# Optimization experiments

Measured on AMD Instinct MI355X. Metric: run time of the kernel, lower is better.

## Reference

```python
import jax, jax.numpy as jnp
import numpy as np

B, C, N = 2, 128, 784  # batch, channels, spatial tokens (28x28)
TEMPERATURE = 11.313708498984761  # sqrt(C)


def setup_inputs() -> dict:
    key = jax.random.key(0)
    kq, kk, kv = jax.random.split(key, 3)
    q = jax.random.normal(kq, (B, C, N), dtype=jnp.float32)
    k = jax.random.normal(kk, (B, C, N), dtype=jnp.float32)
    v = jax.random.normal(kv, (B, C, N), dtype=jnp.float32)
    return {"q": q, "k": k, "v": v}


def reference(q, k, v):
    # dist_func == 'l1' branch of ScaledDotProductAttention (eval mode, dropout=0)
    qs = q / TEMPERATURE                                   # [B, C, Nq]
    # torch: q.unsqueeze(2).repeat -> [B,C,Nk,Nq]; k.unsqueeze(3).repeat -> [B,C,Nk,Nq]
    # broadcast instead of repeat; mean over channel dim 1
    diff = jnp.abs(qs[:, :, None, :] - k[:, :, :, None])   # [B, C, Nk, Nq]
    attn = jnp.mean(diff, axis=1)                          # [B, Nk, Nq]
    attn = jax.nn.softmax(attn, axis=-1)                   # softmax over Nq (last dim)
    # torch.bmm(v, attn.permute(0,2,1)): out[b,c,k] = sum_q v[b,c,q] * attn[b,k,q]
    out = jnp.einsum("bcq,bkq->bck", v, attn)              # [B, C, Nk]
    return (out, attn)
```

## Files before the change

kernel.cpp:

```cpp
#include <hip/hip_runtime.h>
#include <math.h>

constexpr int kB = 2;
constexpr int kC = 128;
constexpr int kN = 784;
constexpr float kInvT = 1.0f / 11.313708498984761f;
constexpr float kInvC = 1.0f / 128.0f;

constexpr size_t kOutElems  = (size_t)kB * kC * kN;
constexpr size_t kAttnElems = (size_t)kB * kN * kN;

__device__ inline float wave_max(float v) {
#pragma unroll
    for (int o = 32; o > 0; o >>= 1) v = fmaxf(v, __shfl_xor(v, o, 64));
    return v;
}
__device__ inline float wave_sum(float v) {
#pragma unroll
    for (int o = 32; o > 0; o >>= 1) v += __shfl_xor(v, o, 64);
    return v;
}

constexpr int TK = 64;
constexpr int TQ = 64;
constexpr int NKT = (kN + TK - 1) / TK;
constexpr int NQT = (kN + TQ - 1) / TQ;
constexpr int CSP = 2;
constexpr int CH = kC / CSP;
constexpr int DSTR = 68;

template <bool USE_WS>
__global__ __launch_bounds__(256) void dist_kernel(const float* __restrict__ qg,
                                                   const float* __restrict__ kg,
                                                   float* __restrict__ D0,
                                                   float* __restrict__ D1) {
    int bid = blockIdx.x;
    const int qt = bid % NQT; bid /= NQT;
    const int kt = bid % NKT; bid /= NKT;
    const int ch = bid & 1;   bid >>= 1;
    const int b  = bid;
    const int k0 = kt * TK;
    const int q0 = qt * TQ;
    const int t  = threadIdx.x;

    __shared__ float ks[CH][DSTR];
    __shared__ float qs[CH][DSTR];

    const float* kb = kg + ((size_t)b * kC + ch * CH) * kN;
    const float* qb = qg + ((size_t)b * kC + ch * CH) * kN;

#pragma unroll
    for (int i = t; i < CH * 16; i += 256) {
        const int c  = i >> 4;
        const int x4 = (i & 15) << 2;
        *reinterpret_cast<float4*>(&ks[c][x4]) =
            *reinterpret_cast<const float4*>(kb + (size_t)c * kN + min(k0 + x4, kN - 4));
        float4 qv = *reinterpret_cast<const float4*>(qb + (size_t)c * kN + min(q0 + x4, kN - 4));
        qv.x *= kInvT; qv.y *= kInvT; qv.z *= kInvT; qv.w *= kInvT;
        *reinterpret_cast<float4*>(&qs[c][x4]) = qv;
    }
    __syncthreads();

    const int qx = (t & 15) << 2;
    const int kx = (t >> 4) << 2;

    float acc[4][4];
#pragma unroll
    for (int i = 0; i < 4; ++i)
#pragma unroll
        for (int j = 0; j < 4; ++j) acc[i][j] = 0.0f;

#pragma unroll 4
    for (int c = 0; c < CH; ++c) {
        const float4 kv = *reinterpret_cast<const float4*>(&ks[c][kx]);
        const float4 qv = *reinterpret_cast<const float4*>(&qs[c][qx]);
        const float kf[4] = {kv.x, kv.y, kv.z, kv.w};
        const float qf[4] = {qv.x, qv.y, qv.z, qv.w};
#pragma unroll
        for (int i = 0; i < 4; ++i)
#pragma unroll
            for (int j = 0; j < 4; ++j)
                acc[i][j] += fabsf(qf[j] - kf[i]);
    }

    const int qcol = q0 + qx;
    if (qcol < kN) {
        float* dst = (USE_WS && ch) ? D1 : D0;
#pragma unroll
        for (int i = 0; i < 4; ++i) {
            const int krow = k0 + kx + i;
            if (krow < kN) {
                const size_t off = ((size_t)b * kN + krow) * kN + qcol;
                if (USE_WS) {
                    *reinterpret_cast<float4*>(dst + off) =
                        make_float4(acc[i][0], acc[i][1], acc[i][2], acc[i][3]);
                } else {
                    atomicAdd(&D0[off + 0], acc[i][0]);
                    atomicAdd(&D0[off + 1], acc[i][1]);
                    atomicAdd(&D0[off + 2], acc[i][2]);
                    atomicAdd(&D0[off + 3], acc[i][3]);
                }
            }
        }
    }
}

template <bool SUM2>
__global__ __launch_bounds__(256) void softmax_kernel(float* __restrict__ A,
                                                      const float* __restrict__ W) {
    const size_t row = (size_t)blockIdx.x * kN;
    float4* A4 = reinterpret_cast<float4*>(A + row);
    const float4* W4 = reinterpret_cast<const float4*>(W + row);
    const int t = threadIdx.x;
    const int lane = t & 63, wid = t >> 6;
    const bool act = t < (kN / 4);
    __shared__ float xred[4];

    float4 x = make_float4(-1e30f, -1e30f, -1e30f, -1e30f);
    if (act) {
        x = A4[t];
        if (SUM2) {
            const float4 w = W4[t];
            x.x += w.x; x.y += w.y; x.z += w.z; x.w += w.w;
        }
    }

    float m = fmaxf(fmaxf(x.x, x.y), fmaxf(x.z, x.w));
    m = wave_max(m);
    if (lane == 0) xred[wid] = m;
    __syncthreads();
    m = fmaxf(fmaxf(xred[0], xred[1]), fmaxf(xred[2], xred[3]));
    __syncthreads();

    float4 p;
    p.x = __expf((x.x - m) * kInvC);
    p.y = __expf((x.y - m) * kInvC);
    p.z = __expf((x.z - m) * kInvC);
    p.w = __expf((x.w - m) * kInvC);
    float lsum = p.x + p.y + p.z + p.w;
    lsum = wave_sum(lsum);
    if (lane == 0) xred[wid] = lsum;
    __syncthreads();
    const float inv = 1.0f / (xred[0] + xred[1] + xred[2] + xred[3]);
    if (act) {
        p.x *= inv; p.y *= inv; p.z *= inv; p.w *= inv;
        A4[t] = p;
    }
}

typedef _Float16 half4v __attribute__((ext_vector_type(4)));
typedef _Float16 half8v __attribute__((ext_vector_type(8)));
typedef float f32x4 __attribute__((ext_vector_type(4)));

constexpr int GM = 64;
constexpr int GN = 64;
constexpr int GK = 128;
constexpr int NCH = (kN + GK - 1) / GK;
constexpr int NKT3 = (kN + GN - 1) / GN;
constexpr int LSTR = 136;

__global__ __launch_bounds__(256) void bmm_mfma(const float* __restrict__ vg,
                                                const float* __restrict__ attn,
                                                float* __restrict__ out) {
    int bid = blockIdx.x;
    const int kt = bid % NKT3; bid /= NKT3;
    const int ct = bid & 1;    bid >>= 1;
    const int b  = bid;
    const int k0 = kt * GN;
    const int c0 = ct * GM;
    const int t  = threadIdx.x;
    const int lane = t & 63;
    const int w = t >> 6;

    __shared__ _Float16 vs[GM][LSTR];
    __shared__ _Float16 as_[GN][LSTR];

    const float* vb = vg + ((size_t)b * kC + c0) * kN;
    const float* ab = attn + (size_t)b * kN * kN;

    const int col4 = t & 31;
    const int rb   = t >> 5;

    float4 pv[8], pa[8];

    auto load_chunk = [&](int chnk) {
        const int qv = chnk * GK + 4 * col4;
        const bool qok = qv < kN;
#pragma unroll
        for (int i = 0; i < 8; ++i) {
            const int row = rb + 8 * i;
            pv[i] = qok ? *reinterpret_cast<const float4*>(vb + (size_t)row * kN + qv)
                        : make_float4(0.f, 0.f, 0.f, 0.f);
            const int krow = k0 + row;
            pa[i] = (qok && krow < kN)
                        ? *reinterpret_cast<const float4*>(ab + (size_t)krow * kN + qv)
                        : make_float4(0.f, 0.f, 0.f, 0.f);
        }
    };

    auto store_chunk = [&]() {
        const int col = 4 * col4;
#pragma unroll
        for (int i = 0; i < 8; ++i) {
            const int row = rb + 8 * i;
            half4v hv = {(_Float16)pv[i].x, (_Float16)pv[i].y,
                         (_Float16)pv[i].z, (_Float16)pv[i].w};
            *reinterpret_cast<half4v*>(&vs[row][col]) = hv;
            half4v ha = {(_Float16)pa[i].x, (_Float16)pa[i].y,
                         (_Float16)pa[i].z, (_Float16)pa[i].w};
            *reinterpret_cast<half4v*>(&as_[row][col]) = ha;
        }
    };

    f32x4 acc[4] = {};

    const int arow = 16 * w + (lane & 15);
    const int brow0 = lane & 15;
    const int kgrp = (lane >> 4) * 8;

    load_chunk(0);
    for (int chnk = 0; chnk < NCH; ++chnk) {
        __syncthreads();
        store_chunk();
        __syncthreads();
        if (chnk + 1 < NCH) load_chunk(chnk + 1);

#pragma unroll
        for (int ks = 0; ks < GK / 32; ++ks) {
            const int koff = ks * 32 + kgrp;
            const half8v av = *reinterpret_cast<const half8v*>(&vs[arow][koff]);
#pragma unroll
            for (int n = 0; n < 4; ++n) {
                const half8v bv =
                    *reinterpret_cast<const half8v*>(&as_[16 * n + brow0][koff]);
                acc[n] = __builtin_amdgcn_mfma_f32_16x16x32_f16(av, bv, acc[n], 0, 0, 0);
            }
        }
    }

    const int crow = c0 + 16 * w + (lane >> 4) * 4;
    const int kc = k0 + (lane & 15);
#pragma unroll
    for (int n = 0; n < 4; ++n) {
        const int kcol = kc + 16 * n;
        if (kcol < kN) {
            float* op = out + ((size_t)b * kC + crow) * kN + kcol;
#pragma unroll
            for (int r = 0; r < 4; ++r) op[(size_t)r * kN] = acc[n][r];
        }
    }
}

extern "C" void kernel_launch(void* const* d_in, const int* in_sizes, int n_in,
                              void* d_out, int out_size, void* d_ws, size_t ws_size,
                              hipStream_t stream) {
    const float* q = (const float*)d_in[0];
    const float* k = (const float*)d_in[1];
    const float* v = (const float*)d_in[2];

    float* out  = (float*)d_out;
    float* attn = out + kOutElems;
    float* D1   = (float*)d_ws;

    const size_t need = kAttnElems * sizeof(float);

    if (ws_size >= need) {
        dist_kernel<true><<<kB * CSP * NKT * NQT, 256, 0, stream>>>(q, k, attn, D1);
        softmax_kernel<true><<<kB * kN, 256, 0, stream>>>(attn, D1);
        bmm_mfma<<<kB * 2 * NKT3, 256, 0, stream>>>(v, attn, out);
    } else {
        hipMemsetAsync(attn, 0, kAttnElems * sizeof(float), stream);
        dist_kernel<false><<<kB * CSP * NKT * NQT, 256, 0, stream>>>(q, k, attn, nullptr);
        softmax_kernel<false><<<kB * kN, 256, 0, stream>>>(attn, attn);
        bmm_mfma<<<kB * 2 * NKT3, 256, 0, stream>>>(v, attn, out);
    }
}
```

Baseline: 107.2 us.

## Split bmm reduction over Nq across blocks and drop LDS staging

The bmm kernel now splits the Nq reduction dimension across blocks, giving 7x more blocks, so the small 52-block grid can fill the GPU. Each wave loads its MFMA operands straight from global memory into registers and converts them to fp16 there, removing the shared-memory staging and barriers. The partial sums are written to a workspace and summed by a new reduce kernel; when there is not enough workspace, atomics into a zeroed output are used instead. In exchange it adds an extra launch and extra global traffic for the partials, and the direct loads read global memory less efficiently.

```diff
diff --git a/kernel.cpp b/kernel.cpp
--- a/kernel.cpp
+++ b/kernel.cpp
@@ -148,107 +148,106 @@
     }
 }
 
-typedef _Float16 half4v __attribute__((ext_vector_type(4)));
 typedef _Float16 half8v __attribute__((ext_vector_type(8)));
 typedef float f32x4 __attribute__((ext_vector_type(4)));
 
-constexpr int GM = 64;
 constexpr int GN = 64;
 constexpr int GK = 128;
-constexpr int NCH = (kN + GK - 1) / GK;
+constexpr int QSP3 = (kN + GK - 1) / GK;
 constexpr int NKT3 = (kN + GN - 1) / GN;
-constexpr int LSTR = 136;
-
+
+__device__ inline half8v to_h8(const float4 a, const float4 b) {
+    half8v h;
+    h[0] = (_Float16)a.x; h[1] = (_Float16)a.y; h[2] = (_Float16)a.z; h[3] = (_Float16)a.w;
+    h[4] = (_Float16)b.x; h[5] = (_Float16)b.y; h[6] = (_Float16)b.z; h[7] = (_Float16)b.w;
+    return h;
+}
+
+template <bool ATOMIC>
 __global__ __launch_bounds__(256) void bmm_mfma(const float* __restrict__ vg,
                                                 const float* __restrict__ attn,
-                                                float* __restrict__ out) {
+                                                float* __restrict__ P) {
     int bid = blockIdx.x;
+    const int qs = bid % QSP3; bid /= QSP3;
     const int kt = bid % NKT3; bid /= NKT3;
     const int ct = bid & 1;    bid >>= 1;
     const int b  = bid;
     const int k0 = kt * GN;
-    const int c0 = ct * GM;
+    const int c0 = ct * 64;
+    const int q0 = qs * GK;
     const int t  = threadIdx.x;
     const int lane = t & 63;
     const int w = t >> 6;
 
-    __shared__ _Float16 vs[GM][LSTR];
-    __shared__ _Float16 as_[GN][LSTR];
-
-    const float* vb = vg + ((size_t)b * kC + c0) * kN;
-    const float* ab = attn + (size_t)b * kN * kN;
-
-    const int col4 = t & 31;
-    const int rb   = t >> 5;
-
-    float4 pv[8], pa[8];
-
-    auto load_chunk = [&](int chnk) {
-        const int qv = chnk * GK + 4 * col4;
-        const bool qok = qv < kN;
-#pragma unroll
-        for (int i = 0; i < 8; ++i) {
-            const int row = rb + 8 * i;
-            pv[i] = qok ? *reinterpret_cast<const float4*>(vb + (size_t)row * kN + qv)
-                        : make_float4(0.f, 0.f, 0.f, 0.f);
-            const int krow = k0 + row;
-            pa[i] = (qok && krow < kN)
-                        ? *reinterpret_cast<const float4*>(ab + (size_t)krow * kN + qv)
-                        : make_float4(0.f, 0.f, 0.f, 0.f);
-        }
-    };
-
-    auto store_chunk = [&]() {
-        const int col = 4 * col4;
-#pragma unroll
-        for (int i = 0; i < 8; ++i) {
-            const int row = rb + 8 * i;
-            half4v hv = {(_Float16)pv[i].x, (_Float16)pv[i].y,
-                         (_Float16)pv[i].z, (_Float16)pv[i].w};
-            *reinterpret_cast<half4v*>(&vs[row][col]) = hv;
-            half4v ha = {(_Float16)pa[i].x, (_Float16)pa[i].y,
-                         (_Float16)pa[i].z, (_Float16)pa[i].w};
-            *reinterpret_cast<half4v*>(&as_[row][col]) = ha;
-        }
-    };
+    const int lrow = lane & 15;
+    const int kgrp = (lane >> 4) * 8;
+
+    const float* vp = vg + (((size_t)b * kC + c0 + 16 * w + lrow) * kN + q0 + kgrp);
+    const float* ap[4];
+#pragma unroll
+    for (int n = 0; n < 4; ++n) {
+        const int krow = min(k0 + 16 * n + lrow, kN - 1);
+        ap[n] = attn + (((size_t)b * kN + krow) * kN + q0 + kgrp);
+    }
 
     f32x4 acc[4] = {};
 
-    const int arow = 16 * w + (lane & 15);
-    const int brow0 = lane & 15;
-    const int kgrp = (lane >> 4) * 8;
-
-    load_chunk(0);
-    for (int chnk = 0; chnk < NCH; ++chnk) {
-        __syncthreads();
-        store_chunk();
-        __syncthreads();
-        if (chnk + 1 < NCH) load_chunk(chnk + 1);
-
+    if (q0 + GK <= kN) {
 #pragma unroll
         for (int ks = 0; ks < GK / 32; ++ks) {
-            const int koff = ks * 32 + kgrp;
-            const half8v av = *reinterpret_cast<const half8v*>(&vs[arow][koff]);
+            const int qb = ks * 32;
+            const half8v av = to_h8(*reinterpret_cast<const float4*>(vp + qb),
+                                    *reinterpret_cast<const float4*>(vp + qb + 4));
 #pragma unroll
             for (int n = 0; n < 4; ++n) {
-                const half8v bv =
-                    *reinterpret_cast<const half8v*>(&as_[16 * n + brow0][koff]);
+                const half8v bv = to_h8(*reinterpret_cast<const float4*>(ap[n] + qb),
+                                        *reinterpret_cast<const float4*>(ap[n] + qb + 4));
                 acc[n] = __builtin_amdgcn_mfma_f32_16x16x32_f16(av, bv, acc[n], 0, 0, 0);
             }
         }
+    } else {
+        const float4 z = make_float4(0.f, 0.f, 0.f, 0.f);
+        const bool ok = (q0 + kgrp) < kN;
+        const half8v av = to_h8(ok ? *reinterpret_cast<const float4*>(vp) : z,
+                                ok ? *reinterpret_cast<const float4*>(vp + 4) : z);
+#pragma unroll
+        for (int n = 0; n < 4; ++n) {
+            const half8v bv = to_h8(ok ? *reinterpret_cast<const float4*>(ap[n]) : z,
+                                    ok ? *reinterpret_cast<const float4*>(ap[n] + 4) : z);
+            acc[n] = __builtin_amdgcn_mfma_f32_16x16x32_f16(av, bv, acc[n], 0, 0, 0);
+        }
     }
 
     const int crow = c0 + 16 * w + (lane >> 4) * 4;
-    const int kc = k0 + (lane & 15);
+    const int kc = k0 + lrow;
 #pragma unroll
     for (int n = 0; n < 4; ++n) {
         const int kcol = kc + 16 * n;
         if (kcol < kN) {
-            float* op = out + ((size_t)b * kC + crow) * kN + kcol;
-#pragma unroll
-            for (int r = 0; r < 4; ++r) op[(size_t)r * kN] = acc[n][r];
-        }
-    }
+            if (ATOMIC) {
+#pragma unroll
+                for (int r = 0; r < 4; ++r)
+                    atomicAdd(&P[((size_t)b * kC + crow + r) * kN + kcol], acc[n][r]);
+            } else {
+                float* op = P + (((size_t)qs * kB + b) * kC + crow) * kN + kcol;
+#pragma unroll
+                for (int r = 0; r < 4; ++r) op[(size_t)r * kN] = acc[n][r];
+            }
+        }
+    }
+}
+
+__global__ __launch_bounds__(256) void reduce_kernel(const float* __restrict__ P,
+                                                     float* __restrict__ out) {
+    const int idx = blockIdx.x * 256 + threadIdx.x;
+    const float4* p = reinterpret_cast<const float4*>(P) + idx;
+    float4 s = p[0];
+#pragma unroll
+    for (int qs = 1; qs < QSP3; ++qs) {
+        const float4 v = p[(size_t)qs * (kOutElems / 4)];
+        s.x += v.x; s.y += v.y; s.z += v.z; s.w += v.w;
+    }
+    reinterpret_cast<float4*>(out)[idx] = s;
 }
 
 extern "C" void kernel_launch(void* const* d_in, const int* in_sizes, int n_in,
@@ -261,17 +260,20 @@
     float* out  = (float*)d_out;
     float* attn = out + kOutElems;
     float* D1   = (float*)d_ws;
-
-    const size_t need = kAttnElems * sizeof(float);
+    float* P    = D1 + kAttnElems;
+
+    const size_t need = (kAttnElems + (size_t)QSP3 * kOutElems) * sizeof(float);
 
     if (ws_size >= need) {
         dist_kernel<true><<<kB * CSP * NKT * NQT, 256, 0, stream>>>(q, k, attn, D1);
         softmax_kernel<true><<<kB * kN, 256, 0, stream>>>(attn, D1);
-        bmm_mfma<<<kB * 2 * NKT3, 256, 0, stream>>>(v, attn, out);
+        bmm_mfma<false><<<kB * 2 * NKT3 * QSP3, 256, 0, stream>>>(v, attn, P);
+        reduce_kernel<<<(int)(kOutElems / 4 / 256), 256, 0, stream>>>(P, out);
     } else {
         hipMemsetAsync(attn, 0, kAttnElems * sizeof(float), stream);
+        hipMemsetAsync(out, 0, kOutElems * sizeof(float), stream);
         dist_kernel<false><<<kB * CSP * NKT * NQT, 256, 0, stream>>>(q, k, attn, nullptr);
         softmax_kernel<false><<<kB * kN, 256, 0, stream>>>(attn, attn);
-        bmm_mfma<<<kB * 2 * NKT3, 256, 0, stream>>>(v, attn, out);
-    }
-}
+        bmm_mfma<true><<<kB * 2 * NKT3 * QSP3, 256, 0, stream>>>(v, attn, out);
+    }
+}
```

Result: faster. 94.84 us (-11.5%).
